# Kernel tuning notes

Measured on AMD Instinct MI355X. Metric: run time of the kernel, lower is better.

The kernel has to match this reference:

```python
import jax, jax.numpy as jnp
import numpy as np

WINDOW_SIZE = 11
SIGMA = 1.5
C1 = 0.01 ** 2
C2 = 0.03 ** 2
LAMBDA_DSSIM = 0.2


def _gaussian_window(channel):
    x = jnp.arange(WINDOW_SIZE, dtype=jnp.float32)
    g = jnp.exp(-((x - WINDOW_SIZE // 2) ** 2) / (2.0 * SIGMA ** 2))
    g = g / g.sum()
    w2d = jnp.outer(g, g)  # [ws, ws]
    # depthwise kernel: [O=C, I=1, ws, ws]
    return jnp.broadcast_to(w2d[None, None], (channel, 1, WINDOW_SIZE, WINDOW_SIZE))


def _dwconv(x, window, channel):
    # x: [1, C, H, W]; same padding ws//2, depthwise (groups=C)
    pad = WINDOW_SIZE // 2
    return jax.lax.conv_general_dilated(
        x, window,
        window_strides=(1, 1),
        padding=((pad, pad), (pad, pad)),
        dimension_numbers=("NCHW", "OIHW", "NCHW"),
        feature_group_count=channel,
    )


def _ssim_mean(img1, img2):
    # img1, img2: [C, H, W]
    channel = img1.shape[0]
    window = _gaussian_window(channel).astype(img1.dtype)
    a = img1[None]  # [1, C, H, W]
    b = img2[None]

    mu1 = _dwconv(a, window, channel)
    mu2 = _dwconv(b, window, channel)
    mu1_sq = mu1 * mu1
    mu2_sq = mu2 * mu2
    mu1_mu2 = mu1 * mu2
    sigma1_sq = _dwconv(a * a, window, channel) - mu1_sq
    sigma2_sq = _dwconv(b * b, window, channel) - mu2_sq
    sigma12 = _dwconv(a * b, window, channel) - mu1_mu2

    ssim_map = ((2 * mu1_mu2 + C1) * (2 * sigma12 + C2)) / (
        (mu1_sq + mu2_sq + C1) * (sigma1_sq + sigma2_sq + C2))
    return ssim_map.mean()


def setup_inputs() -> dict:
    key = jax.random.key(0)
    k1, k2 = jax.random.split(key)
    shape = (3, 2160, 3840)
    pred = jax.random.uniform(k1, shape, dtype=jnp.float32)
    target = jax.random.uniform(k2, shape, dtype=jnp.float32)
    return {"pred": pred, "target": target}


def reference(pred, target):
    l1 = jnp.abs(pred - target).mean()
    ssim_val = _ssim_mean(pred, target)
    return (1.0 - LAMBDA_DSSIM) * l1 + LAMBDA_DSSIM * (1.0 - ssim_val)
```

## Files before the change

kernel.cpp:

```cpp
#include <hip/hip_runtime.h>
#include <math.h>

#define WSZ 11
#define PAD 5
#define TX 32
#define TY 24
#define NY 6
#define IY (TY + 2*PAD)
#define RX 4
#define NTASK (IY * 8)
#define SEG (RX + 2*PAD)
#define RY 3
#define SA 33
#define SB 35

typedef float v2f __attribute__((ext_vector_type(2)));

struct W11 { float w[WSZ]; };

__global__ __launch_bounds__(256, 4) void ssim_l1_kernel(
    const float* __restrict__ pred, const float* __restrict__ targ,
    W11 wt, float2* __restrict__ partials)
{
    constexpr int H = 2160, W = 3840;
    __shared__ float4 sHA[IY][SA];
    __shared__ float  sHB[IY][SB];

    const int c   = blockIdx.z;
    const int gx0 = blockIdx.x * TX;
    const size_t plane = (size_t)H * W;
    const float* p = pred + (size_t)c * plane;
    const float* t = targ + (size_t)c * plane;

    const int tid = threadIdx.x;
    v2f loss_acc = {0.f, 0.f};
    const float C1v = 0.0001f, C2v = 0.0009f;

    const int oxB  = tid & 31;
    const int oy0B = (tid >> 5) * RY;
    const bool xfast = (blockIdx.x >= 1) && (blockIdx.x <= (W / TX) - 2);

    for (int s = 0; s < NY; ++s) {
        const int gy0 = (blockIdx.y * NY + s) * TY;

        for (int task = tid; task < NTASK; task += 256) {
            const int r  = task >> 3;
            const int cx = task & 7;
            const int gy  = gy0 + r - PAD;
            const int gxs = gx0 + cx * RX - PAD;
            const bool rowok = (gy >= 0) && (gy < H);

            float4 P[5], T[5];
            if (rowok && xfast) {
                const float4* p4 = (const float4*)(p + (size_t)gy * W + (gxs - 3));
                const float4* t4 = (const float4*)(t + (size_t)gy * W + (gxs - 3));
                #pragma unroll
                for (int i = 0; i < 5; ++i) { P[i] = p4[i]; T[i] = t4[i]; }
            } else if (rowok) {
                const size_t rowoff = (size_t)gy * W;
                #pragma unroll
                for (int i = 0; i < 5; ++i) {
                    float pe[4], te[4];
                    #pragma unroll
                    for (int q = 0; q < 4; ++q) {
                        int gx = gxs - 3 + 4 * i + q;
                        bool ok = (gx >= 0) && (gx < W);
                        pe[q] = ok ? p[rowoff + gx] : 0.f;
                        te[q] = ok ? t[rowoff + gx] : 0.f;
                    }
                    P[i] = make_float4(pe[0], pe[1], pe[2], pe[3]);
                    T[i] = make_float4(te[0], te[1], te[2], te[3]);
                }
            } else {
                #pragma unroll
                for (int i = 0; i < 5; ++i) {
                    P[i] = make_float4(0.f, 0.f, 0.f, 0.f);
                    T[i] = make_float4(0.f, 0.f, 0.f, 0.f);
                }
            }

            v2f h_ab[RX], h_sq[RX];
            float h_pt[RX];
            #pragma unroll
            for (int j = 0; j < RX; ++j) {
                h_ab[j] = (v2f){0.f, 0.f};
                h_sq[j] = (v2f){0.f, 0.f};
                h_pt[j] = 0.f;
            }
            #pragma unroll
            for (int e = 0; e < SEG; ++e) {
                const int ii = (e + 3) >> 2, qq = (e + 3) & 3;
                const float pe = (qq == 0) ? P[ii].x : (qq == 1) ? P[ii].y
                                : (qq == 2) ? P[ii].z : P[ii].w;
                const float te = (qq == 0) ? T[ii].x : (qq == 1) ? T[ii].y
                                : (qq == 2) ? T[ii].z : T[ii].w;
                v2f vab; vab.x = pe; vab.y = te;
                const v2f vsq = vab * vab;
                const float pt = pe * te;
                #pragma unroll
                for (int j = 0; j < RX; ++j) {
                    const int k = e - j;
                    if (k >= 0 && k < WSZ) {
                        const float wv = wt.w[k];
                        h_ab[j] += wv * vab;
                        h_sq[j] += wv * vsq;
                        h_pt[j] += wv * pt;
                    }
                }
                if (e >= PAD && e < PAD + RX && r >= PAD && r < PAD + TY)
                    loss_acc.y += fabsf(pe - te);
            }
            const int xb = cx * RX;
            #pragma unroll
            for (int j = 0; j < RX; ++j) {
                sHA[r][xb + j] = make_float4(h_ab[j].x, h_ab[j].y,
                                             h_sq[j].x, h_sq[j].y);
                sHB[r][xb + j] = h_pt[j];
            }
        }
        __syncthreads();

        {
            v2f mu[RY], sq[RY];
            float sp[RY];
            #pragma unroll
            for (int j = 0; j < RY; ++j) {
                mu[j] = (v2f){0.f, 0.f};
                sq[j] = (v2f){0.f, 0.f};
                sp[j] = 0.f;
            }
            #pragma unroll
            for (int k = 0; k < RY + 2 * PAD; ++k) {
                const float4 f = sHA[oy0B + k][oxB];
                const float  g = sHB[oy0B + k][oxB];
                v2f fab; fab.x = f.x; fab.y = f.y;
                v2f fsq; fsq.x = f.z; fsq.y = f.w;
                #pragma unroll
                for (int j = 0; j < RY; ++j) {
                    const int kk = k - j;
                    if (kk >= 0 && kk < WSZ) {
                        const float wv = wt.w[kk];
                        mu[j] += wv * fab;
                        sq[j] += wv * fsq;
                        sp[j] += wv * g;
                    }
                }
            }
            #pragma unroll
            for (int j = 0; j < RY; ++j) {
                const float m1 = mu[j].x, m2 = mu[j].y;
                const float mu1s = m1 * m1;
                const float mu2s = m2 * m2;
                const float m12  = m1 * m2;
                const float num = (2.f * m12 + C1v) * (2.f * (sp[j] - m12) + C2v);
                const float den = (mu1s + mu2s + C1v)
                                * ((sq[j].x - mu1s) + (sq[j].y - mu2s) + C2v);
                loss_acc.x += num * __builtin_amdgcn_rcpf(den);
            }
        }
        __syncthreads();
    }

    #pragma unroll
    for (int off = 32; off > 0; off >>= 1) {
        loss_acc.x += __shfl_down(loss_acc.x, off, 64);
        loss_acc.y += __shfl_down(loss_acc.y, off, 64);
    }
    __shared__ float red[2][4];
    const int lane = tid & 63;
    const int wid  = tid >> 6;
    if (lane == 0) { red[0][wid] = loss_acc.x; red[1][wid] = loss_acc.y; }
    __syncthreads();
    if (tid == 0) {
        const float sv = red[0][0] + red[0][1] + red[0][2] + red[0][3];
        const float lv = red[1][0] + red[1][1] + red[1][2] + red[1][3];
        const int bid = (blockIdx.z * gridDim.y + blockIdx.y) * gridDim.x + blockIdx.x;
        partials[bid] = make_float2(sv, lv);
    }
}

__global__ __launch_bounds__(256) void finalize_kernel(
    const float2* __restrict__ partials, int n,
    float* __restrict__ out, double invN)
{
    const int tid = threadIdx.x;
    double s = 0.0, l = 0.0;
    for (int i = tid; i < n; i += 256) {
        float2 v = partials[i];
        s += (double)v.x;
        l += (double)v.y;
    }
    #pragma unroll
    for (int off = 32; off > 0; off >>= 1) {
        s += __shfl_down(s, off, 64);
        l += __shfl_down(l, off, 64);
    }
    __shared__ double rs[4], rl[4];
    const int lane = tid & 63, wid = tid >> 6;
    if (lane == 0) { rs[wid] = s; rl[wid] = l; }
    __syncthreads();
    if (tid == 0) {
        const double st = rs[0] + rs[1] + rs[2] + rs[3];
        const double lt = rl[0] + rl[1] + rl[2] + rl[3];
        out[0] = (float)(0.8 * lt * invN + 0.2 * (1.0 - st * invN));
    }
}

extern "C" void kernel_launch(void* const* d_in, const int* in_sizes, int n_in,
                              void* d_out, int out_size, void* d_ws, size_t ws_size,
                              hipStream_t stream)
{
    const float* pred = (const float*)d_in[0];
    const float* targ = (const float*)d_in[1];
    float* out = (float*)d_out;
    float2* partials = (float2*)d_ws;

    const int C = 3, H = 2160, W = 3840;

    W11 wt;
    double g[WSZ], sg = 0.0;
    for (int i = 0; i < WSZ; ++i) {
        double d = (double)i - (WSZ / 2);
        g[i] = exp(-(d * d) / (2.0 * 1.5 * 1.5));
        sg += g[i];
    }
    for (int i = 0; i < WSZ; ++i) wt.w[i] = (float)(g[i] / sg);

    dim3 grid(W / TX, H / (TY * NY), C);
    ssim_l1_kernel<<<grid, 256, 0, stream>>>(pred, targ, wt, partials);

    const int nblocks = (W / TX) * (H / (TY * NY)) * C;
    double invN = 1.0 / ((double)C * (double)H * (double)W);
    finalize_kernel<<<1, 256, 0, stream>>>(partials, nblocks, out, invN);
}
```

Measured before the change: 307.3 us.

## Reuse overlapping halo rows of horizontal pass across vertical sub-tiles

Across the NY sub-tiles each block walks vertically, the bottom 10 halo rows of horizontal-filtered data are copied in shared memory to the top of the buffer. Only the 24 new rows are loaded and filtered instead of all 34. This removes redundant global loads and horizontal convolution work. It adds a shared-memory copy loop and an extra barrier per sub-tile, and the L1 ownership test is rewritten to use global row bounds.

```diff
diff --git a/kernel.cpp b/kernel.cpp
--- a/kernel.cpp
+++ b/kernel.cpp
@@ -8,7 +8,8 @@
 #define NY 6
 #define IY (TY + 2*PAD)
 #define RX 4
-#define NTASK (IY * 8)
+#define NTASK0 (IY * 8)
+#define NTASK1 (TY * 8)
 #define SEG (RX + 2*PAD)
 #define RY 3
 #define SA 33
@@ -26,8 +27,9 @@
     __shared__ float4 sHA[IY][SA];
     __shared__ float  sHB[IY][SB];
 
-    const int c   = blockIdx.z;
-    const int gx0 = blockIdx.x * TX;
+    const int c    = blockIdx.z;
+    const int gx0  = blockIdx.x * TX;
+    const int base = blockIdx.y * (TY * NY);
     const size_t plane = (size_t)H * W;
     const float* p = pred + (size_t)c * plane;
     const float* t = targ + (size_t)c * plane;
@@ -41,14 +43,26 @@
     const bool xfast = (blockIdx.x >= 1) && (blockIdx.x <= (W / TX) - 2);
 
     for (int s = 0; s < NY; ++s) {
-        const int gy0 = (blockIdx.y * NY + s) * TY;
-
-        for (int task = tid; task < NTASK; task += 256) {
+        if (s > 0) {
+            for (int i = tid; i < 2 * PAD * TX; i += 256) {
+                const int dr = i >> 5, cc = i & 31;
+                sHA[dr][cc] = sHA[dr + TY][cc];
+                sHB[dr][cc] = sHB[dr + TY][cc];
+            }
+            __syncthreads();
+        }
+
+        const int ntask  = (s == 0) ? NTASK0 : NTASK1;
+        const int rowoff = (s == 0) ? 0 : 2 * PAD;
+        const int gyA    = base + TY * s - PAD;
+        for (int task = tid; task < ntask; task += 256) {
             const int r  = task >> 3;
             const int cx = task & 7;
-            const int gy  = gy0 + r - PAD;
+            const int rr = rowoff + r;
+            const int gy = gyA + rr;
             const int gxs = gx0 + cx * RX - PAD;
-            const bool rowok = (gy >= 0) && (gy < H);
+            const bool rowok   = (gy >= 0) && (gy < H);
+            const bool own_row = (gy >= base) && (gy < base + TY * NY);
 
             float4 P[5], T[5];
             if (rowok && xfast) {
@@ -57,7 +71,7 @@
                 #pragma unroll
                 for (int i = 0; i < 5; ++i) { P[i] = p4[i]; T[i] = t4[i]; }
             } else if (rowok) {
-                const size_t rowoff = (size_t)gy * W;
+                const size_t rowoff2 = (size_t)gy * W;
                 #pragma unroll
                 for (int i = 0; i < 5; ++i) {
                     float pe[4], te[4];
@@ -65,8 +79,8 @@
                     for (int q = 0; q < 4; ++q) {
                         int gx = gxs - 3 + 4 * i + q;
                         bool ok = (gx >= 0) && (gx < W);
-                        pe[q] = ok ? p[rowoff + gx] : 0.f;
-                        te[q] = ok ? t[rowoff + gx] : 0.f;
+                        pe[q] = ok ? p[rowoff2 + gx] : 0.f;
+                        te[q] = ok ? t[rowoff2 + gx] : 0.f;
                     }
                     P[i] = make_float4(pe[0], pe[1], pe[2], pe[3]);
                     T[i] = make_float4(te[0], te[1], te[2], te[3]);
@@ -107,15 +121,15 @@
                         h_pt[j] += wv * pt;
                     }
                 }
-                if (e >= PAD && e < PAD + RX && r >= PAD && r < PAD + TY)
+                if (e >= PAD && e < PAD + RX && own_row)
                     loss_acc.y += fabsf(pe - te);
             }
             const int xb = cx * RX;
             #pragma unroll
             for (int j = 0; j < RX; ++j) {
-                sHA[r][xb + j] = make_float4(h_ab[j].x, h_ab[j].y,
-                                             h_sq[j].x, h_sq[j].y);
-                sHB[r][xb + j] = h_pt[j];
+                sHA[rr][xb + j] = make_float4(h_ab[j].x, h_ab[j].y,
+                                              h_sq[j].x, h_sq[j].y);
+                sHB[rr][xb + j] = h_pt[j];
             }
         }
         __syncthreads();
```

Measured after the change: 274.8 us. 1.12x faster.
